# Performance work log

Measured on AMD Instinct MI355X. Metric: run time of the kernel, lower is better.

Reference implementation:

```python
import jax, jax.numpy as jnp
import numpy as np

D_MODEL = 1024
N_HEADS = 16
HEAD_DIM = D_MODEL // N_HEADS
ROPE_BASE = 10000.0


def rope_rot(t, pos):
    # t: [B, L, H, hd], pos: [L] int32 absolute positions. Rotate-half RoPE.
    hd = t.shape[-1]
    inv_freq = 1.0 / (ROPE_BASE ** (jnp.arange(0, hd, 2, dtype=jnp.float32) / hd))
    freqs = pos.astype(jnp.float32)[:, None] * inv_freq[None, :]  # [L, hd/2]
    cos = jnp.cos(freqs)[None, :, None, :]  # [1, L, 1, hd/2]
    sin = jnp.sin(freqs)[None, :, None, :]
    t1, t2 = t[..., : hd // 2], t[..., hd // 2 :]
    return jnp.concatenate([t1 * cos - t2 * sin, t2 * cos + t1 * sin], axis=-1)


def setup_inputs() -> dict:
    key = jax.random.key(0)
    ks = jax.random.split(key, 8)
    B, L, S = 8, 16, 8192
    x = jax.random.normal(ks[0], (B, L, D_MODEL), dtype=jnp.float32)
    cache_k = jax.random.normal(ks[1], (B, S, N_HEADS, HEAD_DIM), dtype=jnp.float32)
    cache_v = jax.random.normal(ks[2], (B, S, N_HEADS, HEAD_DIM), dtype=jnp.float32)
    sc = 1.0 / np.sqrt(D_MODEL)
    qkv_w = jax.random.normal(ks[3], (D_MODEL, 3 * D_MODEL), dtype=jnp.float32) * sc
    qkv_b = jnp.zeros((3 * D_MODEL,), dtype=jnp.float32)
    o_w = jax.random.normal(ks[4], (D_MODEL, D_MODEL), dtype=jnp.float32) * sc
    o_b = jnp.zeros((D_MODEL,), dtype=jnp.float32)
    return {
        "x": x,
        "cache_k": cache_k,
        "cache_v": cache_v,
        "qkv_w": qkv_w,
        "qkv_b": qkv_b,
        "o_w": o_w,
        "o_b": o_b,
        "cache_index": S,
    }


def reference(x, cache_k, cache_v, qkv_w, qkv_b, o_w, o_b, cache_index):
    B, L, _ = x.shape
    qkv = x @ qkv_w + qkv_b  # [B, L, 3*d]
    q, k, v = jnp.split(qkv, 3, axis=-1)
    q = q.reshape(B, L, N_HEADS, HEAD_DIM)
    k = k.reshape(B, L, N_HEADS, HEAD_DIM)
    v = v.reshape(B, L, N_HEADS, HEAD_DIM)
    pos = cache_index + jnp.arange(L, dtype=jnp.int32)
    q = rope_rot(q, pos)
    k = rope_rot(k, pos)
    # streaming: append new k/v to cache (cached entries already RoPE-rotated)
    k_full = jnp.concatenate([cache_k, k], axis=1)  # [B, S+L, H, hd]
    v_full = jnp.concatenate([cache_v, v], axis=1)
    scale = 1.0 / jnp.sqrt(jnp.asarray(HEAD_DIM, dtype=q.dtype))
    scores = jnp.einsum("blhd,bshd->bhls", q, k_full) * scale  # [B, H, L, S+L]
    probs = jax.nn.softmax(scores, axis=-1)  # no mask in original module
    out = jnp.einsum("bhls,bshd->blhd", probs, v_full)
    out = out.reshape(B, L, D_MODEL)
    return out @ o_w + o_b
```

## Files before the change

kernel.cpp:

```cpp
#include <hip/hip_runtime.h>

#define B_ 8
#define L_ 16
#define H_ 16
#define D_ 64
#define DM 1024
#define S_ 8192

__device__ __forceinline__ void gld_lds16(const float* g, float* l) {
  __builtin_amdgcn_global_load_lds(
      (const __attribute__((address_space(1))) void*)g,
      (__attribute__((address_space(3))) void*)l, 16, 0, 0);
}

__global__ void __launch_bounds__(256) gemm_splitk_kernel(
    const float* __restrict__ A, const float* __restrict__ W,
    float* __restrict__ part, int lda, int ldw, int Kchunk)
{
  const int c0 = blockIdx.x * 64;
  const int k0 = blockIdx.y * Kchunk;
  const int t  = threadIdx.x;
  __shared__ float xs[32][132];
  __shared__ float wsm[32][64];
  float acc[8][4];
  #pragma unroll
  for (int i = 0; i < 8; ++i)
    #pragma unroll
    for (int j = 0; j < 4; ++j) acc[i][j] = 0.f;
  const int rg = t >> 4, cg = t & 15;
  const int r0 = rg * 8, ct0 = cg * 4;
  for (int ks = 0; ks < Kchunk; ks += 32) {
    __syncthreads();
    #pragma unroll
    for (int i = 0; i < 4; ++i) {
      int fi = t + i * 256;
      int r = fi >> 3, kq = fi & 7;
      float4 v = *(const float4*)(A + (size_t)r * lda + k0 + ks + kq * 4);
      xs[kq*4+0][r] = v.x; xs[kq*4+1][r] = v.y;
      xs[kq*4+2][r] = v.z; xs[kq*4+3][r] = v.w;
    }
    #pragma unroll
    for (int i = 0; i < 2; ++i) {
      int si = t + i * 256;
      int kk = si >> 4, cq = si & 15;
      *(float4*)&wsm[kk][cq*4] =
          *(const float4*)(W + (size_t)(k0 + ks + kk) * ldw + c0 + cq * 4);
    }
    __syncthreads();
    #pragma unroll
    for (int kk = 0; kk < 32; ++kk) {
      float a[8], bb[4];
      *(float4*)&a[0] = *(const float4*)&xs[kk][r0];
      *(float4*)&a[4] = *(const float4*)&xs[kk][r0 + 4];
      *(float4*)&bb[0] = *(const float4*)&wsm[kk][ct0];
      #pragma unroll
      for (int ii = 0; ii < 8; ++ii)
        #pragma unroll
        for (int jj = 0; jj < 4; ++jj)
          acc[ii][jj] = fmaf(a[ii], bb[jj], acc[ii][jj]);
    }
  }
  float* po = part + (size_t)blockIdx.y * 128 * ldw;
  #pragma unroll
  for (int ii = 0; ii < 8; ++ii)
    #pragma unroll
    for (int jj = 0; jj < 4; ++jj)
      po[(size_t)(r0 + ii) * ldw + c0 + ct0 + jj] = acc[ii][jj];
}

__global__ void ropefuse_kernel(const float* __restrict__ part,
                                const float* __restrict__ bias,
                                const int* __restrict__ cidx,
                                float* __restrict__ qh, float* __restrict__ kn,
                                float* __restrict__ vn)
{
  int gt = blockIdx.x * 256 + threadIdx.x;
  int i = gt & 31, l = (gt >> 5) & 15, h = (gt >> 9) & 15, b = gt >> 13;
  int row = b * L_ + l;
  const int PS = 128 * 3072;
  const float* pr = part + (size_t)row * 3072;
  int cq = h * 64 + i;
  int cols[6] = {cq, cq + 32, 1024 + cq, 1024 + cq + 32, 2048 + cq, 2048 + cq + 32};
  float v[6];
  #pragma unroll
  for (int c = 0; c < 6; ++c) {
    float s = bias[cols[c]];
    #pragma unroll
    for (int ks = 0; ks < 4; ++ks) s += pr[(size_t)ks * PS + cols[c]];
    v[c] = s;
  }
  int pos = cidx[0] + l;
  float inv = exp2f((float)i * (-13.287712379549449f / 32.0f));
  float fr = (float)pos * inv;
  float sn, cs;
  sincosf(fr, &sn, &cs);
  int ob = ((b * H_ + h) * L_ + l) * 64;
  qh[ob + i]      = (v[0] * cs - v[1] * sn) * 0.125f;
  qh[ob + 32 + i] = (v[1] * cs + v[0] * sn) * 0.125f;
  kn[ob + i]      = v[2] * cs - v[3] * sn;
  kn[ob + 32 + i] = v[3] * cs + v[2] * sn;
  vn[ob + i]      = v[4];
  vn[ob + 32 + i] = v[5];
}

__global__ void __launch_bounds__(256, 4) attn_partial_kernel(
    const float* __restrict__ qh, const float* __restrict__ kc,
    const float* __restrict__ vc, float* __restrict__ opart,
    float* __restrict__ lpart)
{
  const int bh = blockIdx.x;
  const int chunk = blockIdx.y;
  const int b = bh >> 4, h = bh & 15;
  const int tid = threadIdx.x;
  const int w = tid >> 6, lane = tid & 63;
  __shared__ float kt[2][32 * 64];
  __shared__ float vt[2][32 * 64];
  __shared__ float ql[16 * 64];
  __shared__ float pl[16 * 32];
  {
    int l = tid >> 4, sl = tid & 15;
    *(float4*)&ql[l * 64 + sl * 4] = *(const float4*)&qh[(size_t)(bh * 16 + l) * 64 + sl * 4];
  }
  const int Lg = w * 4;
  const int rowi = lane >> 4, p = lane & 15;
  float l_run[4];
  float4 op[4];
  #pragma unroll
  for (int li = 0; li < 4; ++li) {
    l_run[li] = 0.f;
    op[li].x = op[li].y = op[li].z = op[li].w = 0.f;
  }
  const size_t base = (size_t)b * S_ * DM + (size_t)h * 64;
  const int s_base = chunk * 1024;

  auto issue = [&](int tt, int buf) {
    const int st = s_base + tt * 32;
    #pragma unroll
    for (int i = 0; i < 2; ++i) {
      const int r0w = w * 8 + i * 4;
      const int r = r0w + rowi;
      const int jk = p ^ (r & 7);
      gld_lds16(kc + base + (size_t)(st + r) * DM + jk * 4, &kt[buf][r0w * 64]);
      gld_lds16(vc + base + (size_t)(st + r) * DM + p * 4,  &vt[buf][r0w * 64]);
    }
  };

  issue(0, 0);
  __syncthreads();

  const int sr = lane & 31, dh = lane >> 5;
  const int sh = lane >> 4, dq = lane & 15;

  for (int tt = 0; tt < 32; ++tt) {
    const int cb = tt & 1;
    if (tt < 31) {
      issue(tt + 1, cb ^ 1);
      asm volatile("s_waitcnt vmcnt(4)" ::: "memory");
    } else {
      asm volatile("s_waitcnt vmcnt(0)" ::: "memory");
    }
    __builtin_amdgcn_sched_barrier(0);
    __builtin_amdgcn_s_barrier();

    float sc[4] = {0.f, 0.f, 0.f, 0.f};
    #pragma unroll
    for (int dc = 0; dc < 8; ++dc) {
      int j = dh * 8 + dc;
      int pp = j ^ (sr & 7);
      float4 kv = *(const float4*)&kt[cb][sr * 64 + pp * 4];
      #pragma unroll
      for (int li = 0; li < 4; ++li) {
        float4 qv = *(const float4*)&ql[(Lg + li) * 64 + j * 4];
        sc[li] += kv.x * qv.x + kv.y * qv.y + kv.z * qv.z + kv.w * qv.w;
      }
    }
    #pragma unroll
    for (int li = 0; li < 4; ++li) {
      float s = sc[li] + __shfl_xor(sc[li], 32);
      float pex = __expf(s);
      l_run[li] += pex;
      pl[(Lg + li) * 32 + sr] = pex;
    }
    #pragma unroll
    for (int jj = 0; jj < 8; ++jj) {
      int s = sh * 8 + jj;
      float4 vv = *(const float4*)&vt[cb][s * 64 + dq * 4];
      #pragma unroll
      for (int li = 0; li < 4; ++li) {
        float pp = pl[(Lg + li) * 32 + s];
        op[li].x = fmaf(pp, vv.x, op[li].x);
        op[li].y = fmaf(pp, vv.y, op[li].y);
        op[li].z = fmaf(pp, vv.z, op[li].z);
        op[li].w = fmaf(pp, vv.w, op[li].w);
      }
    }
    __builtin_amdgcn_s_barrier();
  }

  #pragma unroll
  for (int li = 0; li < 4; ++li) {
    #pragma unroll
    for (int d = 16; d < 64; d <<= 1) {
      op[li].x += __shfl_xor(op[li].x, d);
      op[li].y += __shfl_xor(op[li].y, d);
      op[li].z += __shfl_xor(op[li].z, d);
      op[li].w += __shfl_xor(op[li].w, d);
    }
    float lr = l_run[li];
    #pragma unroll
    for (int d = 1; d < 64; d <<= 1) lr += __shfl_xor(lr, d);
    if (lane < 16)
      *(float4*)&opart[(((size_t)chunk * 128 + bh) * 16 + Lg + li) * 64 + dq * 4] = op[li];
    if (lane == 0)
      lpart[(chunk * 128 + bh) * 16 + Lg + li] = lr * 0.5f;
  }
}

__global__ void __launch_bounds__(64) combine_kernel(
    const float* __restrict__ qh, const float* __restrict__ kn,
    const float* __restrict__ vn, const float* __restrict__ opart,
    const float* __restrict__ lpart, float* __restrict__ attn)
{
  const int bh = blockIdx.x;
  const int b = bh >> 4, h = bh & 15;
  const int lane = threadIdx.x;
  __shared__ float qb[1024], kb[1024], vb[1024];
  __shared__ float scn[16][16];
  for (int l = 0; l < 16; ++l) {
    qb[l * 64 + lane] = qh[(size_t)(bh * 16 + l) * 64 + lane];
    kb[l * 64 + lane] = kn[(size_t)(bh * 16 + l) * 64 + lane];
    vb[l * 64 + lane] = vn[(size_t)(bh * 16 + l) * 64 + lane];
  }
  __syncthreads();
  {
    int l = lane >> 2, sp0 = (lane & 3) * 4;
    for (int jj = 0; jj < 4; ++jj) {
      int sp = sp0 + jj;
      float a = 0.f;
      for (int d = 0; d < 64; ++d) a += qb[l * 64 + d] * kb[sp * 64 + d];
      scn[l][sp] = a;
    }
  }
  __syncthreads();
  for (int l = 0; l < 16; ++l) {
    float den = 0.f, od = 0.f;
    #pragma unroll
    for (int c = 0; c < 8; ++c) {
      den += lpart[(c * 128 + bh) * 16 + l];
      od  += opart[(((size_t)c * 128 + bh) * 16 + l) * 64 + lane];
    }
    for (int sp = 0; sp < 16; ++sp) {
      float pex = __expf(scn[l][sp]);
      den += pex;
      od += pex * vb[sp * 64 + lane];
    }
    attn[((size_t)(b * 16 + l) * 16 + h) * 64 + lane] = od / den;
  }
}

__global__ void reduce_out_kernel(const float* __restrict__ part2,
                                  const float* __restrict__ ob,
                                  float* __restrict__ out)
{
  int idx = blockIdx.x * 256 + threadIdx.x;
  int c = idx & 1023;
  float s = ob[c];
  #pragma unroll
  for (int ks = 0; ks < 8; ++ks) s += part2[(size_t)ks * 131072 + idx];
  out[idx] = s;
}

extern "C" void kernel_launch(void* const* d_in, const int* in_sizes, int n_in,
                              void* d_out, int out_size, void* d_ws, size_t ws_size,
                              hipStream_t stream) {
  (void)in_sizes; (void)n_in; (void)out_size; (void)ws_size;
  const float* x       = (const float*)d_in[0];
  const float* cache_k = (const float*)d_in[1];
  const float* cache_v = (const float*)d_in[2];
  const float* qkv_w   = (const float*)d_in[3];
  const float* qkv_b   = (const float*)d_in[4];
  const float* o_w     = (const float*)d_in[5];
  const float* o_b     = (const float*)d_in[6];
  const int*   cidx    = (const int*)d_in[7];
  float* out = (float*)d_out;

  float* ws    = (float*)d_ws;
  float* part1 = ws;
  float* qh    = part1 + 1572864;
  float* kn    = qh + 131072;
  float* vn    = kn + 131072;
  float* opart = vn + 131072;
  float* lpart = opart + 1048576;
  float* attn  = lpart + 16384;
  float* part2 = attn + 131072;

  gemm_splitk_kernel<<<dim3(48, 4), 256, 0, stream>>>(x, qkv_w, part1, 1024, 3072, 256);
  ropefuse_kernel<<<256, 256, 0, stream>>>(part1, qkv_b, cidx, qh, kn, vn);
  attn_partial_kernel<<<dim3(128, 8), 256, 0, stream>>>(qh, cache_k, cache_v,
                                                        opart, lpart);
  combine_kernel<<<128, 64, 0, stream>>>(qh, kn, vn, opart, lpart, attn);
  gemm_splitk_kernel<<<dim3(16, 8), 256, 0, stream>>>(attn, o_w, part2, 1024, 1024, 128);
  reduce_out_kernel<<<512, 256, 0, stream>>>(part2, o_b, out);
}
```

Baseline: 246.1 us.

## Restructure attention partial kernel to load full contiguous KV rows across all heads

The attention partial kernel now assigns each 512-thread block one batch and a 128-position chunk covering all 16 heads. It streams whole contiguous 4KB K/V rows into LDS instead of strided 256-byte per-head slices, and each thread keeps one query half-row in registers. The split is raised from 8 to 64 chunks, so the combine kernel, now split across 4 query groups per head, must reduce 64 partials. Workspace buffers are aliased to hold the larger partial output. The aim is better DRAM coalescing on the cache stream, at the cost of more partial-sum traffic and higher register pressure.

```diff
diff --git a/kernel.cpp b/kernel.cpp
--- a/kernel.cpp
+++ b/kernel.cpp
@@ -103,58 +103,51 @@
   vn[ob + 32 + i] = v[5];
 }
 
-__global__ void __launch_bounds__(256, 4) attn_partial_kernel(
+__global__ void __launch_bounds__(512, 4) attn_partial_kernel(
     const float* __restrict__ qh, const float* __restrict__ kc,
     const float* __restrict__ vc, float* __restrict__ opart,
     float* __restrict__ lpart)
 {
-  const int bh = blockIdx.x;
-  const int chunk = blockIdx.y;
-  const int b = bh >> 4, h = bh & 15;
-  const int tid = threadIdx.x;
+  const int chunk = blockIdx.x;
+  const int b     = blockIdx.y;
+  const int tid   = threadIdx.x;
   const int w = tid >> 6, lane = tid & 63;
-  __shared__ float kt[2][32 * 64];
-  __shared__ float vt[2][32 * 64];
-  __shared__ float ql[16 * 64];
-  __shared__ float pl[16 * 32];
+  const int h = tid >> 5, l = (tid >> 1) & 15, dh = tid & 1;
+  __shared__ float kv[2][8192];
+
+  float4 qr[8];
   {
-    int l = tid >> 4, sl = tid & 15;
-    *(float4*)&ql[l * 64 + sl * 4] = *(const float4*)&qh[(size_t)(bh * 16 + l) * 64 + sl * 4];
-  }
-  const int Lg = w * 4;
-  const int rowi = lane >> 4, p = lane & 15;
-  float l_run[4];
-  float4 op[4];
-  #pragma unroll
-  for (int li = 0; li < 4; ++li) {
-    l_run[li] = 0.f;
-    op[li].x = op[li].y = op[li].z = op[li].w = 0.f;
-  }
-  const size_t base = (size_t)b * S_ * DM + (size_t)h * 64;
-  const int s_base = chunk * 1024;
-
-  auto issue = [&](int tt, int buf) {
-    const int st = s_base + tt * 32;
-    #pragma unroll
-    for (int i = 0; i < 2; ++i) {
-      const int r0w = w * 8 + i * 4;
-      const int r = r0w + rowi;
-      const int jk = p ^ (r & 7);
-      gld_lds16(kc + base + (size_t)(st + r) * DM + jk * 4, &kt[buf][r0w * 64]);
-      gld_lds16(vc + base + (size_t)(st + r) * DM + p * 4,  &vt[buf][r0w * 64]);
-    }
+    const float* qb = qh + (size_t)b * 16384 + (size_t)tid * 32;
+    #pragma unroll
+    for (int j = 0; j < 8; ++j)
+      qr[j] = *(const float4*)(qb + ((j ^ (dh << 2)) << 2));
+  }
+  float4 o[8];
+  #pragma unroll
+  for (int j = 0; j < 8; ++j) o[j].x = o[j].y = o[j].z = o[j].w = 0.f;
+  float l_run = 0.f;
+
+  const size_t kbase = (size_t)b * S_ * DM;
+  const int st0 = chunk * 128;
+
+  auto issue = [&](int t, int buf) {
+    const int r = st0 + t * 4 + (w & 3);
+    const float* src = (w < 4 ? kc : vc) + kbase + (size_t)r * DM + lane * 4;
+    float* dst = &kv[buf][(w < 4 ? 0 : 4096) + (w & 3) * 1024];
+    #pragma unroll
+    for (int i = 0; i < 4; ++i)
+      gld_lds16(src + i * 256, dst + i * 256);
   };
 
   issue(0, 0);
+  asm volatile("s_waitcnt vmcnt(0)" ::: "memory");
   __syncthreads();
 
-  const int sr = lane & 31, dh = lane >> 5;
-  const int sh = lane >> 4, dq = lane & 15;
-
-  for (int tt = 0; tt < 32; ++tt) {
-    const int cb = tt & 1;
-    if (tt < 31) {
-      issue(tt + 1, cb ^ 1);
+  const int koff = h * 64 + dh * 32;
+  for (int t = 0; t < 32; ++t) {
+    const int cb = t & 1;
+    if (t < 31) {
+      issue(t + 1, cb ^ 1);
       asm volatile("s_waitcnt vmcnt(4)" ::: "memory");
     } else {
       asm volatile("s_waitcnt vmcnt(0)" ::: "memory");
@@ -162,58 +155,37 @@
     __builtin_amdgcn_sched_barrier(0);
     __builtin_amdgcn_s_barrier();
 
-    float sc[4] = {0.f, 0.f, 0.f, 0.f};
-    #pragma unroll
-    for (int dc = 0; dc < 8; ++dc) {
-      int j = dh * 8 + dc;
-      int pp = j ^ (sr & 7);
-      float4 kv = *(const float4*)&kt[cb][sr * 64 + pp * 4];
+    #pragma unroll
+    for (int r = 0; r < 4; ++r) {
+      const float* kr = &kv[cb][r * 1024 + koff];
+      const float* vr = &kv[cb][4096 + r * 1024 + koff];
+      float sc = 0.f;
       #pragma unroll
-      for (int li = 0; li < 4; ++li) {
-        float4 qv = *(const float4*)&ql[(Lg + li) * 64 + j * 4];
-        sc[li] += kv.x * qv.x + kv.y * qv.y + kv.z * qv.z + kv.w * qv.w;
+      for (int j = 0; j < 8; ++j) {
+        float4 k4 = *(const float4*)(kr + ((j ^ (dh << 2)) << 2));
+        sc += k4.x * qr[j].x + k4.y * qr[j].y + k4.z * qr[j].z + k4.w * qr[j].w;
       }
-    }
-    #pragma unroll
-    for (int li = 0; li < 4; ++li) {
-      float s = sc[li] + __shfl_xor(sc[li], 32);
+      float s = sc + __shfl_xor(sc, 1);
       float pex = __expf(s);
-      l_run[li] += pex;
-      pl[(Lg + li) * 32 + sr] = pex;
-    }
-    #pragma unroll
-    for (int jj = 0; jj < 8; ++jj) {
-      int s = sh * 8 + jj;
-      float4 vv = *(const float4*)&vt[cb][s * 64 + dq * 4];
+      l_run += pex;
       #pragma unroll
-      for (int li = 0; li < 4; ++li) {
-        float pp = pl[(Lg + li) * 32 + s];
-        op[li].x = fmaf(pp, vv.x, op[li].x);
-        op[li].y = fmaf(pp, vv.y, op[li].y);
-        op[li].z = fmaf(pp, vv.z, op[li].z);
-        op[li].w = fmaf(pp, vv.w, op[li].w);
+      for (int j = 0; j < 8; ++j) {
+        float4 v4 = *(const float4*)(vr + ((j ^ (dh << 2)) << 2));
+        o[j].x = fmaf(pex, v4.x, o[j].x);
+        o[j].y = fmaf(pex, v4.y, o[j].y);
+        o[j].z = fmaf(pex, v4.z, o[j].z);
+        o[j].w = fmaf(pex, v4.w, o[j].w);
       }
     }
     __builtin_amdgcn_s_barrier();
   }
 
-  #pragma unroll
-  for (int li = 0; li < 4; ++li) {
-    #pragma unroll
-    for (int d = 16; d < 64; d <<= 1) {
-      op[li].x += __shfl_xor(op[li].x, d);
-      op[li].y += __shfl_xor(op[li].y, d);
-      op[li].z += __shfl_xor(op[li].z, d);
-      op[li].w += __shfl_xor(op[li].w, d);
-    }
-    float lr = l_run[li];
-    #pragma unroll
-    for (int d = 1; d < 64; d <<= 1) lr += __shfl_xor(lr, d);
-    if (lane < 16)
-      *(float4*)&opart[(((size_t)chunk * 128 + bh) * 16 + Lg + li) * 64 + dq * 4] = op[li];
-    if (lane == 0)
-      lpart[(chunk * 128 + bh) * 16 + Lg + li] = lr * 0.5f;
-  }
+  const size_t ob = (((size_t)(b * 64 + chunk) * 16 + h) * 16 + l) * 64;
+  #pragma unroll
+  for (int j = 0; j < 8; ++j)
+    *(float4*)&opart[ob + dh * 32 + ((j ^ (dh << 2)) << 2)] = o[j];
+  if (dh == 0)
+    lpart[((b * 64 + chunk) * 16 + h) * 16 + l] = l_run;
 }
 
 __global__ void __launch_bounds__(64) combine_kernel(
@@ -223,34 +195,37 @@
 {
   const int bh = blockIdx.x;
   const int b = bh >> 4, h = bh & 15;
+  const int l0 = blockIdx.y * 4;
   const int lane = threadIdx.x;
-  __shared__ float qb[1024], kb[1024], vb[1024];
-  __shared__ float scn[16][16];
-  for (int l = 0; l < 16; ++l) {
-    qb[l * 64 + lane] = qh[(size_t)(bh * 16 + l) * 64 + lane];
-    kb[l * 64 + lane] = kn[(size_t)(bh * 16 + l) * 64 + lane];
-    vb[l * 64 + lane] = vn[(size_t)(bh * 16 + l) * 64 + lane];
+  __shared__ float kb[1024], vb[1024], qb[256];
+  __shared__ float scn[4][16];
+  for (int i = 0; i < 16; ++i) {
+    kb[i * 64 + lane] = kn[(size_t)(bh * 16 + i) * 64 + lane];
+    vb[i * 64 + lane] = vn[(size_t)(bh * 16 + i) * 64 + lane];
+  }
+  {
+    int ll = lane >> 4, sl = lane & 15;
+    *(float4*)&qb[ll * 64 + sl * 4] =
+        *(const float4*)&qh[(size_t)(bh * 16 + l0 + ll) * 64 + sl * 4];
   }
   __syncthreads();
   {
-    int l = lane >> 2, sp0 = (lane & 3) * 4;
-    for (int jj = 0; jj < 4; ++jj) {
-      int sp = sp0 + jj;
-      float a = 0.f;
-      for (int d = 0; d < 64; ++d) a += qb[l * 64 + d] * kb[sp * 64 + d];
-      scn[l][sp] = a;
-    }
+    int ll = lane >> 4, sp = lane & 15;
+    float a = 0.f;
+    for (int d = 0; d < 64; ++d) a += qb[ll * 64 + d] * kb[sp * 64 + d];
+    scn[ll][sp] = a;
   }
   __syncthreads();
-  for (int l = 0; l < 16; ++l) {
+  for (int ll = 0; ll < 4; ++ll) {
+    const int l = l0 + ll;
     float den = 0.f, od = 0.f;
-    #pragma unroll
-    for (int c = 0; c < 8; ++c) {
-      den += lpart[(c * 128 + bh) * 16 + l];
-      od  += opart[(((size_t)c * 128 + bh) * 16 + l) * 64 + lane];
-    }
+    for (int c = 0; c < 64; ++c) {
+      den += lpart[((b * 64 + c) * 16 + h) * 16 + l];
+      od  += opart[(((size_t)(b * 64 + c) * 16 + h) * 16 + l) * 64 + lane];
+    }
+    #pragma unroll
     for (int sp = 0; sp < 16; ++sp) {
-      float pex = __expf(scn[l][sp]);
+      float pex = __expf(scn[ll][sp]);
       den += pex;
       od += pex * vb[sp * 64 + lane];
     }
@@ -285,20 +260,21 @@
   float* out = (float*)d_out;
 
   float* ws    = (float*)d_ws;
-  float* part1 = ws;
-  float* qh    = part1 + 1572864;
+  float* big   = ws;
+  float* part1 = big;
+  float* opart = big;
+  float* part2 = big;
+  float* qh    = big + 8388608;
   float* kn    = qh + 131072;
   float* vn    = kn + 131072;
-  float* opart = vn + 131072;
-  float* lpart = opart + 1048576;
-  float* attn  = lpart + 16384;
-  float* part2 = attn + 131072;
+  float* lpart = vn + 131072;
+  float* attn  = lpart + 131072;
 
   gemm_splitk_kernel<<<dim3(48, 4), 256, 0, stream>>>(x, qkv_w, part1, 1024, 3072, 256);
   ropefuse_kernel<<<256, 256, 0, stream>>>(part1, qkv_b, cidx, qh, kn, vn);
-  attn_partial_kernel<<<dim3(128, 8), 256, 0, stream>>>(qh, cache_k, cache_v,
-                                                        opart, lpart);
-  combine_kernel<<<128, 64, 0, stream>>>(qh, kn, vn, opart, lpart, attn);
+  attn_partial_kernel<<<dim3(64, 8), 512, 0, stream>>>(qh, cache_k, cache_v,
+                                                       opart, lpart);
+  combine_kernel<<<dim3(128, 4), 64, 0, stream>>>(qh, kn, vn, opart, lpart, attn);
   gemm_splitk_kernel<<<dim3(16, 8), 256, 0, stream>>>(attn, o_w, part2, 1024, 1024, 128);
   reduce_out_kernel<<<512, 256, 0, stream>>>(part2, o_b, out);
 }
```

Result: faster. 199.7 us (-18.9%).
